# Kernel optimization log

Measured on AMD Instinct MI355X. Metric: run time of the kernel, lower is better.

Reference implementation:

```python
import jax, jax.numpy as jnp
import numpy as np

THETA = 10000.0
NUM_HEADS = 16


def _rope_tables(seq_len, d_k, dtype):
    exponent = jnp.arange(d_k // 2, dtype=jnp.float32) * (2.0 / d_k)
    inv_freq = THETA ** (-exponent)                      # (d_k/2,)
    pos = jnp.arange(seq_len, dtype=jnp.float32)
    angles = pos[:, None] * inv_freq[None, :]            # (n, d_k/2)
    return jnp.cos(angles).astype(dtype), jnp.sin(angles).astype(dtype)


def _apply_rope(x, cos, sin):
    # x: (..., n, d_k); interleaved pair convention: pairs are (x[...,2i], x[...,2i+1])
    x1 = x[..., 0::2]
    x2 = x[..., 1::2]
    r1 = x1 * cos - x2 * sin
    r2 = x1 * sin + x2 * cos
    return jnp.stack([r1, r2], axis=-1).reshape(x.shape)


def setup_inputs() -> dict:
    key = jax.random.key(0)
    ks = jax.random.split(key, 5)
    B, N, D = 2, 4096, 1024
    std = (2.0 / (D + D)) ** 0.5
    return {
        "x": jax.random.normal(ks[0], (B, N, D), dtype=jnp.float32),
        "Wq": jax.random.normal(ks[1], (D, D), dtype=jnp.float32) * std,
        "Wk": jax.random.normal(ks[2], (D, D), dtype=jnp.float32) * std,
        "Wv": jax.random.normal(ks[3], (D, D), dtype=jnp.float32) * std,
        "Wo": jax.random.normal(ks[4], (D, D), dtype=jnp.float32) * std,
    }


def reference(x, Wq, Wk, Wv, Wo):
    B, N, D = x.shape
    H = NUM_HEADS
    d_k = D // H

    def proj(W):
        y = jnp.einsum('oi,bni->bno', W, x)
        return y.reshape(B, N, H, d_k).transpose(0, 2, 1, 3)  # (b,h,n,d)

    Q, K, V = proj(Wq), proj(Wk), proj(Wv)

    cos, sin = _rope_tables(N, d_k, x.dtype)
    Q = _apply_rope(Q, cos, sin)
    K = _apply_rope(K, cos, sin)

    scores = jnp.einsum('bhnd,bhmd->bhnm', Q, K) / jnp.sqrt(jnp.asarray(d_k, x.dtype))
    causal = jnp.tril(jnp.ones((N, N), dtype=bool))
    scores = jnp.where(causal, scores, -jnp.inf)
    attn = jax.nn.softmax(scores, axis=-1)
    out = jnp.einsum('bhnm,bhmd->bhnd', attn, V)          # (b,h,n,d)
    out = out.transpose(0, 2, 1, 3).reshape(B, N, D)
    return jnp.einsum('oi,bni->bno', Wo, out)
```

## Files before the change

kernel.cpp:

```cpp
#include <hip/hip_runtime.h>
#include <hip/hip_bf16.h>
#include <stdint.h>

typedef __attribute__((ext_vector_type(8))) short short8;
typedef __attribute__((ext_vector_type(4))) float f32x4;
typedef __attribute__((ext_vector_type(2))) unsigned uint32x2;

#define NSEQ 4096
#define DMODEL 1024
#define MROWS 8192

__device__ __forceinline__ unsigned short f2bf(float f) {
  union { float f; unsigned u; } v; v.f = f;
  unsigned r = v.u + 0x7fffu + ((v.u >> 16) & 1u);
  return (unsigned short)(r >> 16);
}

__device__ __forceinline__ unsigned pk2(float lo, float hi) {
  unsigned short a = __bfloat16_as_ushort(__float2bfloat16(lo));
  unsigned short b = __bfloat16_as_ushort(__float2bfloat16(hi));
  return ((unsigned)b << 16) | (unsigned)a;
}

__device__ __forceinline__ void gload16(const unsigned short* g, unsigned short* l) {
  __builtin_amdgcn_global_load_lds(
      (const __attribute__((address_space(1))) unsigned int*)g,
      (__attribute__((address_space(3))) unsigned int*)l, 16, 0, 0);
}

__device__ __forceinline__ void pexch(unsigned x, unsigned y, unsigned& w_lo, unsigned& w_hi) {
  uint32x2 t = __builtin_amdgcn_permlane32_swap(x, y, false, false);
  uint32x2 u = __builtin_amdgcn_permlane16_swap(t[0], t[1], false, false);
  w_lo = u[0];
  w_hi = u[1];
}

__global__ void k_conv(const float* __restrict__ src, unsigned short* __restrict__ dst) {
  int i = (blockIdx.x * 256 + threadIdx.x) * 4;
  float4 v = *(const float4*)(src + i);
  ushort4 o;
  o.x = f2bf(v.x); o.y = f2bf(v.y); o.z = f2bf(v.z); o.w = f2bf(v.w);
  *(ushort4*)(dst + i) = o;
}

__global__ void k_convw(const float* __restrict__ s0, const float* __restrict__ s1,
                        const float* __restrict__ s2, const float* __restrict__ s3,
                        unsigned short* __restrict__ dst) {
  int z = blockIdx.x >> 10;
  const float* src = (z == 0) ? s0 : (z == 1) ? s1 : (z == 2) ? s2 : s3;
  float sc = (z == 0) ? 0.18033688011112042f : 1.0f;
  int i = ((blockIdx.x & 1023) * 256 + threadIdx.x) * 4;
  float4 v = *(const float4*)(src + i);
  ushort4 o;
  o.x = f2bf(v.x * sc); o.y = f2bf(v.y * sc); o.z = f2bf(v.z * sc); o.w = f2bf(v.w * sc);
  *(ushort4*)(dst + (size_t)z * 1048576 + i) = o;
}

__global__ void k_rope_tab(float* __restrict__ cosT, float* __restrict__ sinT) {
  int i = blockIdx.x * 256 + threadIdx.x;
  int pos = i >> 5, j = i & 31;
  float invf = exp2f(-(float)j * 0.41524101186092029f);
  float ang = (float)pos * invf;
  cosT[i] = cosf(ang);
  sinT[i] = sinf(ang);
}

__global__ __launch_bounds__(256) void k_gemm_bt(
    const unsigned short* __restrict__ A,
    const unsigned short* __restrict__ Bw,
    unsigned short* __restrict__ obf,
    unsigned short* __restrict__ Vt,
    float* __restrict__ of32,
    const float* __restrict__ cosT, const float* __restrict__ sinT,
    int K, int modeArg) {
  const int N = DMODEL;
  const int q8 = gridDim.x >> 3;
  const int wg = (blockIdx.x & 7) * q8 + (blockIdx.x >> 3);
  const int z = wg >> 9;
  const int rr = wg & 511;
  const int bn = rr & 7, bm = rr >> 3;
  const int mode = (modeArg < 0) ? z : modeArg;
  const unsigned short* Bz = Bw + (size_t)z * DMODEL * K;
  unsigned short* oz = (obf && mode <= 1) ? (obf + (size_t)z * MROWS * DMODEL) : nullptr;

  const int t = threadIdx.x;
  const int w = t >> 6, lane = t & 63;
  const int wr = w >> 1, wc = w & 1;
  const int lr = lane & 15, lg = lane >> 4;

  __shared__ __align__(16) unsigned short SM[2][128 * 64];
  unsigned short* Al = SM[0];
  unsigned short* Bl = SM[1];

  const unsigned short* Ab = A + (size_t)bm * 128 * K;
  const unsigned short* Bb = Bz + (size_t)bn * 128 * K;
  const int trow = t >> 3, tcol = (t & 7) * 8;

  f32x4 acc[4][4] = {};

  for (int k0 = 0; k0 < K; k0 += 64) {
#pragma unroll
    for (int c = 0; c < 4; ++c) {
      gload16(Ab + (size_t)(c * 32 + trow) * K + k0 + tcol, &Al[c * 2048 + t * 8]);
      gload16(Bb + (size_t)(c * 32 + trow) * K + k0 + tcol, &Bl[c * 2048 + t * 8]);
    }
    asm volatile("s_waitcnt vmcnt(0)" ::: "memory");
    __syncthreads();
#pragma unroll
    for (int kk = 0; kk < 2; ++kk) {
      short8 af[4], bfr[4];
#pragma unroll
      for (int mi = 0; mi < 4; ++mi)
        af[mi] = *(const short8*)&Al[(wr * 64 + mi * 16 + lr) * 64 + kk * 32 + lg * 8];
#pragma unroll
      for (int ni = 0; ni < 4; ++ni)
        bfr[ni] = *(const short8*)&Bl[(wc * 64 + ni * 16 + lr) * 64 + kk * 32 + lg * 8];
#pragma unroll
      for (int mi = 0; mi < 4; ++mi)
#pragma unroll
        for (int ni = 0; ni < 4; ++ni)
          acc[mi][ni] = __builtin_amdgcn_mfma_f32_16x16x32_bf16(af[mi], bfr[ni], acc[mi][ni], 0, 0, 0);
    }
    __syncthreads();
  }

  if (mode <= 1 || mode == 3) {
    float* Cf = (float*)&SM[0][0];
#pragma unroll
    for (int half = 0; half < 2; ++half) {
      if (half) __syncthreads();
      if (wr == half) {
#pragma unroll
        for (int mi = 0; mi < 4; ++mi)
#pragma unroll
          for (int ni = 0; ni < 4; ++ni)
#pragma unroll
            for (int r = 0; r < 4; ++r) {
              int row = mi * 16 + lg * 4 + r;
              int col = (wc * 64 + ni * 16 + lr) ^ (lg << 3);
              Cf[row * 128 + col] = acc[mi][ni][r];
            }
      }
      __syncthreads();
      int pr = t >> 2;
      int gm = bm * 128 + half * 64 + pr;
      int xorv = ((pr >> 2) & 3) << 3;
      if (mode == 3) {
        float* orow = of32 + (size_t)gm * N + bn * 128;
#pragma unroll
        for (int k = 0; k < 4; ++k) {
          int c0 = (t & 3) * 8 + k * 32;
          int cs = c0 ^ xorv;
          float4 va = *(const float4*)&Cf[pr * 128 + cs];
          float4 vb = *(const float4*)&Cf[pr * 128 + cs + 4];
          *(float4*)(orow + c0) = va;
          *(float4*)(orow + c0 + 4) = vb;
        }
      } else {
        int pos = gm & (NSEQ - 1);
        const float* cB = cosT + pos * 32;
        const float* sB = sinT + pos * 32;
        unsigned short* orow = oz + (size_t)gm * N + bn * 128;
#pragma unroll
        for (int k = 0; k < 4; ++k) {
          int c0 = (t & 3) * 8 + k * 32;
          int cs = c0 ^ xorv;
          float4 va = *(const float4*)&Cf[pr * 128 + cs];
          float4 vb = *(const float4*)&Cf[pr * 128 + cs + 4];
          int j0 = (c0 & 63) >> 1;
          float4 cv = *(const float4*)&cB[j0];
          float4 sv = *(const float4*)&sB[j0];
          uint4 o;
          o.x = pk2(va.x * cv.x - va.y * sv.x, va.x * sv.x + va.y * cv.x);
          o.y = pk2(va.z * cv.y - va.w * sv.y, va.z * sv.y + va.w * cv.y);
          o.z = pk2(vb.x * cv.z - vb.y * sv.z, vb.x * sv.z + vb.y * cv.z);
          o.w = pk2(vb.z * cv.w - vb.w * sv.w, vb.z * sv.w + vb.w * cv.w);
          *(uint4*)(orow + c0) = o;
        }
      }
    }
  } else {
#pragma unroll
    for (int mi = 0; mi < 4; ++mi)
#pragma unroll
      for (int ni = 0; ni < 4; ++ni) {
        int gm0 = bm * 128 + wr * 64 + mi * 16 + lg * 4;
        int gn = bn * 128 + wc * 64 + ni * 16 + lr;
        int b = gm0 >> 12, n = gm0 & (NSEQ - 1);
        int h = gn >> 6, d = gn & 63;
        uint2 u;
        u.x = pk2(acc[mi][ni][0], acc[mi][ni][1]);
        u.y = pk2(acc[mi][ni][2], acc[mi][ni][3]);
        *(uint2*)(Vt + ((size_t)((b * 16 + h) * 64 + d)) * NSEQ + n) = u;
      }
  }
}

__global__ __launch_bounds__(256, 2) void k_attn8(
    const unsigned short* __restrict__ Qb,
    const unsigned short* __restrict__ Kb,
    const unsigned short* __restrict__ Vtg,
    unsigned short* __restrict__ AO) {
  const int id = blockIdx.x;
  const int bh = id & 31;
  const int pq = id >> 5;
  const int b = bh >> 4, h = bh & 15;
  const int t = threadIdx.x;
  const int w = t >> 6, lane = t & 63;
  const int lr = lane & 15, hi4 = lane >> 4;
  const size_t rowbase = (size_t)b * NSEQ;

  __shared__ __align__(16) unsigned short Kl[2][64 * 64];
  __shared__ __align__(16) unsigned short Vl[2][64 * 64];
  __shared__ __align__(16) unsigned short Pl[4][16 * 64];

  const int pswz = (lr & 7) << 3;

  short8 ones;
#pragma unroll
  for (int i = 0; i < 8; ++i) ones[i] = (short)0x3F80;

#define STAGE(buf, kv0)                                                                   \
  {                                                                                       \
    _Pragma("unroll")                                                                     \
    for (int it = 0; it < 2; ++it) {                                                      \
      int c = t + it * 256;                                                               \
      int row = c >> 3, sg = (c & 7) ^ (row & 7);                                         \
      gload16(Kb + (rowbase + (kv0) + row) * DMODEL + h * 64 + sg * 8, &Kl[buf][c * 8]);  \
      gload16(Vtg + ((size_t)bh * 64 + row) * NSEQ + (kv0) + sg * 8, &Vl[buf][c * 8]);    \
    }                                                                                     \
  }

#pragma unroll
  for (int qi = 0; qi < 2; ++qi) {
    const int qt = qi ? pq : (31 - pq);
    const int q0w = qt * 128 + w * 32;

    short8 qf[2][2];
#pragma unroll
    for (int sub = 0; sub < 2; ++sub) {
      const unsigned short* qp = Qb + (rowbase + q0w + sub * 16 + lr) * DMODEL + h * 64 + hi4 * 8;
#pragma unroll
      for (int s = 0; s < 2; ++s)
        qf[sub][s] = *(const short8*)(qp + s * 32);
    }

    f32x4 oacc[2][4] = {};
    f32x4 lacc[2] = {};
    const int nkv = (qt + 1) * 2;

    STAGE(0, 0);
    asm volatile("s_waitcnt vmcnt(0)" ::: "memory");
    __syncthreads();

    for (int ib = 0; ib < nkv; ++ib) {
      const int kv0 = ib * 64, cur = ib & 1;
      if (ib + 1 < nkv) STAGE(cur ^ 1, kv0 + 64);

      if (kv0 <= q0w + 31) {
        short8 Kf[4][2], Vf[2][4];
#pragma unroll
        for (int t4 = 0; t4 < 4; ++t4)
#pragma unroll
          for (int s = 0; s < 2; ++s)
            Kf[t4][s] = *(const short8*)&Kl[cur][(t4 * 16 + lr) * 64 + (((s * 4 + hi4) ^ (lr & 7)) * 8)];
#pragma unroll
        for (int c = 0; c < 2; ++c)
#pragma unroll
          for (int dt = 0; dt < 4; ++dt)
            Vf[c][dt] = *(const short8*)&Vl[cur][(dt * 16 + lr) * 64 + (((c * 4 + hi4) ^ (lr & 7)) * 8)];

#pragma unroll
        for (int sub = 0; sub < 2; ++sub) {
          const int qs = q0w + sub * 16;
          const int qlane = qs + lr;
          f32x4 sa[4];
          const f32x4 zz = {0.f, 0.f, 0.f, 0.f};
          __builtin_amdgcn_s_setprio(1);
#pragma unroll
          for (int t4 = 0; t4 < 4; ++t4) {
            f32x4 x = __builtin_amdgcn_mfma_f32_16x16x32_bf16(Kf[t4][0], qf[sub][0], zz, 0, 0, 0);
            sa[t4] = __builtin_amdgcn_mfma_f32_16x16x32_bf16(Kf[t4][1], qf[sub][1], x, 0, 0, 0);
          }
          __builtin_amdgcn_s_setprio(0);
          if (kv0 + 63 > qs) {
#pragma unroll
            for (int t4 = 0; t4 < 4; ++t4)
#pragma unroll
              for (int r = 0; r < 4; ++r)
                if (kv0 + t4 * 16 + hi4 * 4 + r > qlane) sa[t4][r] = -1e30f;
          }
#pragma unroll
          for (int t4 = 0; t4 < 4; ++t4)
#pragma unroll
            for (int r = 0; r < 4; ++r)
              sa[t4][r] = __builtin_amdgcn_exp2f(sa[t4][r]);

          unsigned a0 = pk2(sa[0][0], sa[0][1]), a1 = pk2(sa[0][2], sa[0][3]);
          unsigned a2 = pk2(sa[1][0], sa[1][1]), a3 = pk2(sa[1][2], sa[1][3]);
          unsigned a4 = pk2(sa[2][0], sa[2][1]), a5 = pk2(sa[2][2], sa[2][3]);
          unsigned a6 = pk2(sa[3][0], sa[3][1]), a7 = pk2(sa[3][2], sa[3][3]);
          unsigned w0, w1, w2, w3, x0, x1, x2, x3;
          pexch(a0, a2, w0, w2);
          pexch(a1, a3, w1, w3);
          pexch(a4, a6, x0, x2);
          pexch(a5, a7, x1, x3);
          union { uint4 u; short8 s; } P0, P1;
          P0.u.x = w0; P0.u.y = w1; P0.u.z = w2; P0.u.w = w3;
          P1.u.x = x0; P1.u.y = x1; P1.u.z = x2; P1.u.w = x3;
          short8 pf0 = P0.s;
          short8 pf1 = P1.s;

          __builtin_amdgcn_s_setprio(1);
#pragma unroll
          for (int dt = 0; dt < 4; ++dt) {
            oacc[sub][dt] = __builtin_amdgcn_mfma_f32_16x16x32_bf16(Vf[0][dt], pf0, oacc[sub][dt], 0, 0, 0);
            oacc[sub][dt] = __builtin_amdgcn_mfma_f32_16x16x32_bf16(Vf[1][dt], pf1, oacc[sub][dt], 0, 0, 0);
          }
          lacc[sub] = __builtin_amdgcn_mfma_f32_16x16x32_bf16(ones, pf0, lacc[sub], 0, 0, 0);
          lacc[sub] = __builtin_amdgcn_mfma_f32_16x16x32_bf16(ones, pf1, lacc[sub], 0, 0, 0);
          __builtin_amdgcn_s_setprio(0);
        }
      }
      asm volatile("s_waitcnt vmcnt(0)" ::: "memory");
      __syncthreads();
    }

#pragma unroll
    for (int sub = 0; sub < 2; ++sub) {
      float inv = 1.f / lacc[sub][0];
#pragma unroll
      for (int dt = 0; dt < 4; ++dt) {
        uint2 u;
        u.x = pk2(oacc[sub][dt][0] * inv, oacc[sub][dt][1] * inv);
        u.y = pk2(oacc[sub][dt][2] * inv, oacc[sub][dt][3] * inv);
        *(uint2*)&Pl[w][lr * 64 + ((dt * 16 + hi4 * 4) ^ pswz)] = u;
      }
      asm volatile("s_waitcnt lgkmcnt(0)" ::: "memory");
      __builtin_amdgcn_sched_barrier(0);
      int q2 = lane >> 2, ch = (lane & 3) * 16;
      int qswz = (q2 & 7) << 3;
      uint4 r0 = *(const uint4*)&Pl[w][q2 * 64 + (ch ^ qswz)];
      uint4 r1 = *(const uint4*)&Pl[w][q2 * 64 + ((ch + 8) ^ qswz)];
      unsigned short* op = AO + (rowbase + q0w + sub * 16 + q2) * DMODEL + h * 64 + ch;
      *(uint4*)op = r0;
      *(uint4*)(op + 8) = r1;
      __syncthreads();
    }
  }
}

extern "C" void kernel_launch(void* const* d_in, const int* in_sizes, int n_in,
                              void* d_out, int out_size, void* d_ws, size_t ws_size,
                              hipStream_t stream) {
  const float* x  = (const float*)d_in[0];
  const float* Wq = (const float*)d_in[1];
  const float* Wk = (const float*)d_in[2];
  const float* Wv = (const float*)d_in[3];
  const float* Wo = (const float*)d_in[4];
  float* out = (float*)d_out;
  char* ws = (char*)d_ws;

  unsigned short* xb  = (unsigned short*)(ws);
  unsigned short* Wb  = (unsigned short*)(ws + 16777216);
  unsigned short* Qb  = (unsigned short*)(ws + 25165824);
  unsigned short* Kb  = Qb + 8388608;
  unsigned short* Vtg = (unsigned short*)(ws + 58720256);
  unsigned short* AO  = (unsigned short*)(ws + 75497472);
  float* cosT = (float*)(ws + 92274688);
  float* sinT = (float*)(ws + 92798976);

  k_conv<<<8192, 256, 0, stream>>>(x, xb);
  k_convw<<<4096, 256, 0, stream>>>(Wq, Wk, Wv, Wo, Wb);
  k_rope_tab<<<512, 256, 0, stream>>>(cosT, sinT);

  k_gemm_bt<<<1536, 256, 0, stream>>>(xb, Wb, Qb, Vtg, nullptr, cosT, sinT, DMODEL, -1);

  k_attn8<<<512, 256, 0, stream>>>(Qb, Kb, Vtg, AO);

  k_gemm_bt<<<512, 256, 0, stream>>>(AO, Wb + 3145728, nullptr, nullptr, out, cosT, sinT, DMODEL, 3);
}
```

Measured before the change: 226.7 us.

## Use 256-row query tiles per attention block to raise K/V reuse

The attention kernel now gives each block one 256-row query tile (64 rows per wave) instead of two paired 128-row tiles. Each staged 64-row K/V tile therefore serves twice as many query rows, which halves shared-memory staging and global K/V traffic. Heavy tiles are dispatched first to soften the causal load imbalance. The costs are more accumulator and P-fragment registers and idle waves on the diagonal tiles. The bf16 packing helper also switches to a manual round-to-nearest-even conversion.

```diff
diff --git a/kernel.cpp b/kernel.cpp
--- a/kernel.cpp
+++ b/kernel.cpp
@@ -17,9 +17,7 @@
 }
 
 __device__ __forceinline__ unsigned pk2(float lo, float hi) {
-  unsigned short a = __bfloat16_as_ushort(__float2bfloat16(lo));
-  unsigned short b = __bfloat16_as_ushort(__float2bfloat16(hi));
-  return ((unsigned)b << 16) | (unsigned)a;
+  return ((unsigned)f2bf(hi) << 16) | (unsigned)f2bf(lo);
 }
 
 __device__ __forceinline__ void gload16(const unsigned short* g, unsigned short* l) {
@@ -196,18 +194,19 @@
   }
 }
 
-__global__ __launch_bounds__(256, 2) void k_attn8(
+__global__ __launch_bounds__(256, 2) void k_attn10(
     const unsigned short* __restrict__ Qb,
     const unsigned short* __restrict__ Kb,
     const unsigned short* __restrict__ Vtg,
     unsigned short* __restrict__ AO) {
   const int id = blockIdx.x;
   const int bh = id & 31;
-  const int pq = id >> 5;
+  const int qt = 15 - (id >> 5);
   const int b = bh >> 4, h = bh & 15;
   const int t = threadIdx.x;
   const int w = t >> 6, lane = t & 63;
   const int lr = lane & 15, hi4 = lane >> 4;
+  const int q0 = qt * 256 + w * 64;
   const size_t rowbase = (size_t)b * NSEQ;
 
   __shared__ __align__(16) unsigned short Kl[2][64 * 64];
@@ -231,122 +230,123 @@
     }                                                                                     \
   }
 
-#pragma unroll
-  for (int qi = 0; qi < 2; ++qi) {
-    const int qt = qi ? pq : (31 - pq);
-    const int q0w = qt * 128 + w * 32;
-
-    short8 qf[2][2];
-#pragma unroll
-    for (int sub = 0; sub < 2; ++sub) {
-      const unsigned short* qp = Qb + (rowbase + q0w + sub * 16 + lr) * DMODEL + h * 64 + hi4 * 8;
-#pragma unroll
-      for (int s = 0; s < 2; ++s)
-        qf[sub][s] = *(const short8*)(qp + s * 32);
-    }
-
-    f32x4 oacc[2][4] = {};
-    f32x4 lacc[2] = {};
-    const int nkv = (qt + 1) * 2;
-
-    STAGE(0, 0);
+  short8 qf[4][2];
+#pragma unroll
+  for (int sub = 0; sub < 4; ++sub) {
+    const unsigned short* qp = Qb + (rowbase + q0 + sub * 16 + lr) * DMODEL + h * 64 + hi4 * 8;
+#pragma unroll
+    for (int s = 0; s < 2; ++s)
+      qf[sub][s] = *(const short8*)(qp + s * 32);
+  }
+
+  f32x4 oacc[4][4] = {};
+  f32x4 lacc[4] = {};
+  const int nkv = (qt + 1) * 4;
+
+  STAGE(0, 0);
+  asm volatile("s_waitcnt vmcnt(0)" ::: "memory");
+  __syncthreads();
+
+  for (int ib = 0; ib < nkv; ++ib) {
+    const int kv0 = ib * 64, cur = ib & 1;
+    if (ib + 1 < nkv) STAGE(cur ^ 1, kv0 + 64);
+
+    if (kv0 <= q0 + 63) {
+      short8 Kf[4][2];
+#pragma unroll
+      for (int t4 = 0; t4 < 4; ++t4)
+#pragma unroll
+        for (int s = 0; s < 2; ++s)
+          Kf[t4][s] = *(const short8*)&Kl[cur][(t4 * 16 + lr) * 64 + (((s * 4 + hi4) ^ (lr & 7)) * 8)];
+
+      short8 pf[4][2];
+#pragma unroll
+      for (int sub = 0; sub < 4; ++sub) {
+        const int qs = q0 + sub * 16;
+        const int qlane = qs + lr;
+        f32x4 sa[4];
+        const f32x4 zz = {0.f, 0.f, 0.f, 0.f};
+        __builtin_amdgcn_s_setprio(1);
+#pragma unroll
+        for (int t4 = 0; t4 < 4; ++t4) {
+          f32x4 x = __builtin_amdgcn_mfma_f32_16x16x32_bf16(Kf[t4][0], qf[sub][0], zz, 0, 0, 0);
+          sa[t4] = __builtin_amdgcn_mfma_f32_16x16x32_bf16(Kf[t4][1], qf[sub][1], x, 0, 0, 0);
+        }
+        __builtin_amdgcn_s_setprio(0);
+        if (kv0 + 63 > qs) {
+#pragma unroll
+          for (int t4 = 0; t4 < 4; ++t4)
+#pragma unroll
+            for (int r = 0; r < 4; ++r)
+              if (kv0 + t4 * 16 + hi4 * 4 + r > qlane) sa[t4][r] = -1e30f;
+        }
+#pragma unroll
+        for (int t4 = 0; t4 < 4; ++t4)
+#pragma unroll
+          for (int r = 0; r < 4; ++r)
+            sa[t4][r] = __builtin_amdgcn_exp2f(sa[t4][r]);
+
+        unsigned a0 = pk2(sa[0][0], sa[0][1]), a1 = pk2(sa[0][2], sa[0][3]);
+        unsigned a2 = pk2(sa[1][0], sa[1][1]), a3 = pk2(sa[1][2], sa[1][3]);
+        unsigned a4 = pk2(sa[2][0], sa[2][1]), a5 = pk2(sa[2][2], sa[2][3]);
+        unsigned a6 = pk2(sa[3][0], sa[3][1]), a7 = pk2(sa[3][2], sa[3][3]);
+        unsigned w0, w1, w2, w3, x0, x1, x2, x3;
+        pexch(a0, a2, w0, w2);
+        pexch(a1, a3, w1, w3);
+        pexch(a4, a6, x0, x2);
+        pexch(a5, a7, x1, x3);
+        union { uint4 u; short8 s; } P0, P1;
+        P0.u.x = w0; P0.u.y = w1; P0.u.z = w2; P0.u.w = w3;
+        P1.u.x = x0; P1.u.y = x1; P1.u.z = x2; P1.u.w = x3;
+        pf[sub][0] = P0.s;
+        pf[sub][1] = P1.s;
+      }
+
+      short8 Vf[2][4];
+#pragma unroll
+      for (int c = 0; c < 2; ++c)
+#pragma unroll
+        for (int dt = 0; dt < 4; ++dt)
+          Vf[c][dt] = *(const short8*)&Vl[cur][(dt * 16 + lr) * 64 + (((c * 4 + hi4) ^ (lr & 7)) * 8)];
+
+      __builtin_amdgcn_s_setprio(1);
+#pragma unroll
+      for (int sub = 0; sub < 4; ++sub) {
+#pragma unroll
+        for (int dt = 0; dt < 4; ++dt) {
+          oacc[sub][dt] = __builtin_amdgcn_mfma_f32_16x16x32_bf16(Vf[0][dt], pf[sub][0], oacc[sub][dt], 0, 0, 0);
+          oacc[sub][dt] = __builtin_amdgcn_mfma_f32_16x16x32_bf16(Vf[1][dt], pf[sub][1], oacc[sub][dt], 0, 0, 0);
+        }
+        lacc[sub] = __builtin_amdgcn_mfma_f32_16x16x32_bf16(ones, pf[sub][0], lacc[sub], 0, 0, 0);
+        lacc[sub] = __builtin_amdgcn_mfma_f32_16x16x32_bf16(ones, pf[sub][1], lacc[sub], 0, 0, 0);
+      }
+      __builtin_amdgcn_s_setprio(0);
+    }
     asm volatile("s_waitcnt vmcnt(0)" ::: "memory");
     __syncthreads();
-
-    for (int ib = 0; ib < nkv; ++ib) {
-      const int kv0 = ib * 64, cur = ib & 1;
-      if (ib + 1 < nkv) STAGE(cur ^ 1, kv0 + 64);
-
-      if (kv0 <= q0w + 31) {
-        short8 Kf[4][2], Vf[2][4];
-#pragma unroll
-        for (int t4 = 0; t4 < 4; ++t4)
-#pragma unroll
-          for (int s = 0; s < 2; ++s)
-            Kf[t4][s] = *(const short8*)&Kl[cur][(t4 * 16 + lr) * 64 + (((s * 4 + hi4) ^ (lr & 7)) * 8)];
-#pragma unroll
-        for (int c = 0; c < 2; ++c)
-#pragma unroll
-          for (int dt = 0; dt < 4; ++dt)
-            Vf[c][dt] = *(const short8*)&Vl[cur][(dt * 16 + lr) * 64 + (((c * 4 + hi4) ^ (lr & 7)) * 8)];
-
-#pragma unroll
-        for (int sub = 0; sub < 2; ++sub) {
-          const int qs = q0w + sub * 16;
-          const int qlane = qs + lr;
-          f32x4 sa[4];
-          const f32x4 zz = {0.f, 0.f, 0.f, 0.f};
-          __builtin_amdgcn_s_setprio(1);
-#pragma unroll
-          for (int t4 = 0; t4 < 4; ++t4) {
-            f32x4 x = __builtin_amdgcn_mfma_f32_16x16x32_bf16(Kf[t4][0], qf[sub][0], zz, 0, 0, 0);
-            sa[t4] = __builtin_amdgcn_mfma_f32_16x16x32_bf16(Kf[t4][1], qf[sub][1], x, 0, 0, 0);
-          }
-          __builtin_amdgcn_s_setprio(0);
-          if (kv0 + 63 > qs) {
-#pragma unroll
-            for (int t4 = 0; t4 < 4; ++t4)
-#pragma unroll
-              for (int r = 0; r < 4; ++r)
-                if (kv0 + t4 * 16 + hi4 * 4 + r > qlane) sa[t4][r] = -1e30f;
-          }
-#pragma unroll
-          for (int t4 = 0; t4 < 4; ++t4)
-#pragma unroll
-            for (int r = 0; r < 4; ++r)
-              sa[t4][r] = __builtin_amdgcn_exp2f(sa[t4][r]);
-
-          unsigned a0 = pk2(sa[0][0], sa[0][1]), a1 = pk2(sa[0][2], sa[0][3]);
-          unsigned a2 = pk2(sa[1][0], sa[1][1]), a3 = pk2(sa[1][2], sa[1][3]);
-          unsigned a4 = pk2(sa[2][0], sa[2][1]), a5 = pk2(sa[2][2], sa[2][3]);
-          unsigned a6 = pk2(sa[3][0], sa[3][1]), a7 = pk2(sa[3][2], sa[3][3]);
-          unsigned w0, w1, w2, w3, x0, x1, x2, x3;
-          pexch(a0, a2, w0, w2);
-          pexch(a1, a3, w1, w3);
-          pexch(a4, a6, x0, x2);
-          pexch(a5, a7, x1, x3);
-          union { uint4 u; short8 s; } P0, P1;
-          P0.u.x = w0; P0.u.y = w1; P0.u.z = w2; P0.u.w = w3;
-          P1.u.x = x0; P1.u.y = x1; P1.u.z = x2; P1.u.w = x3;
-          short8 pf0 = P0.s;
-          short8 pf1 = P1.s;
-
-          __builtin_amdgcn_s_setprio(1);
-#pragma unroll
-          for (int dt = 0; dt < 4; ++dt) {
-            oacc[sub][dt] = __builtin_amdgcn_mfma_f32_16x16x32_bf16(Vf[0][dt], pf0, oacc[sub][dt], 0, 0, 0);
-            oacc[sub][dt] = __builtin_amdgcn_mfma_f32_16x16x32_bf16(Vf[1][dt], pf1, oacc[sub][dt], 0, 0, 0);
-          }
-          lacc[sub] = __builtin_amdgcn_mfma_f32_16x16x32_bf16(ones, pf0, lacc[sub], 0, 0, 0);
-          lacc[sub] = __builtin_amdgcn_mfma_f32_16x16x32_bf16(ones, pf1, lacc[sub], 0, 0, 0);
-          __builtin_amdgcn_s_setprio(0);
-        }
-      }
-      asm volatile("s_waitcnt vmcnt(0)" ::: "memory");
-      __syncthreads();
-    }
-
-#pragma unroll
-    for (int sub = 0; sub < 2; ++sub) {
-      float inv = 1.f / lacc[sub][0];
-#pragma unroll
-      for (int dt = 0; dt < 4; ++dt) {
-        uint2 u;
-        u.x = pk2(oacc[sub][dt][0] * inv, oacc[sub][dt][1] * inv);
-        u.y = pk2(oacc[sub][dt][2] * inv, oacc[sub][dt][3] * inv);
-        *(uint2*)&Pl[w][lr * 64 + ((dt * 16 + hi4 * 4) ^ pswz)] = u;
-      }
-      asm volatile("s_waitcnt lgkmcnt(0)" ::: "memory");
-      __builtin_amdgcn_sched_barrier(0);
-      int q2 = lane >> 2, ch = (lane & 3) * 16;
-      int qswz = (q2 & 7) << 3;
-      uint4 r0 = *(const uint4*)&Pl[w][q2 * 64 + (ch ^ qswz)];
-      uint4 r1 = *(const uint4*)&Pl[w][q2 * 64 + ((ch + 8) ^ qswz)];
-      unsigned short* op = AO + (rowbase + q0w + sub * 16 + q2) * DMODEL + h * 64 + ch;
-      *(uint4*)op = r0;
-      *(uint4*)(op + 8) = r1;
-      __syncthreads();
-    }
+  }
+
+#pragma unroll
+  for (int sub = 0; sub < 4; ++sub) {
+    float inv = 1.f / lacc[sub][0];
+#pragma unroll
+    for (int dt = 0; dt < 4; ++dt) {
+      uint2 u;
+      u.x = pk2(oacc[sub][dt][0] * inv, oacc[sub][dt][1] * inv);
+      u.y = pk2(oacc[sub][dt][2] * inv, oacc[sub][dt][3] * inv);
+      *(uint2*)&Pl[w][lr * 64 + ((dt * 16 + hi4 * 4) ^ pswz)] = u;
+    }
+    asm volatile("s_waitcnt lgkmcnt(0)" ::: "memory");
+    __builtin_amdgcn_sched_barrier(0);
+    int q2 = lane >> 2, ch = (lane & 3) * 16;
+    int qswz = (q2 & 7) << 3;
+    uint4 r0 = *(const uint4*)&Pl[w][q2 * 64 + (ch ^ qswz)];
+    uint4 r1 = *(const uint4*)&Pl[w][q2 * 64 + ((ch + 8) ^ qswz)];
+    unsigned short* op = AO + (rowbase + q0 + sub * 16 + q2) * DMODEL + h * 64 + ch;
+    *(uint4*)op = r0;
+    *(uint4*)(op + 8) = r1;
+    asm volatile("s_waitcnt lgkmcnt(0)" ::: "memory");
+    __builtin_amdgcn_sched_barrier(0);
   }
 }
 
@@ -376,7 +376,7 @@
 
   k_gemm_bt<<<1536, 256, 0, stream>>>(xb, Wb, Qb, Vtg, nullptr, cosT, sinT, DMODEL, -1);
 
-  k_attn8<<<512, 256, 0, stream>>>(Qb, Kb, Vtg, AO);
+  k_attn10<<<512, 256, 0, stream>>>(Qb, Kb, Vtg, AO);
 
   k_gemm_bt<<<512, 256, 0, stream>>>(AO, Wb + 3145728, nullptr, nullptr, out, cosT, sinT, DMODEL, 3);
 }
```

Measured after the change: 258.9 us. 1.14x slower.

## Restructure attention into 512-thread blocks covering 256-query tiles

Applied to the files above, without the earlier changes.

The attention kernel now uses 8 waves per block, each block owning one 256-row query tile. Previously a 4-wave block processed two 128-row tiles one after another, paired for load balance. Each K/V tile staged in LDS is now shared by twice as many query rows, cutting global K/V traffic and per-tile staging overhead, and the sequential two-tile loop goes away. Causal balance now comes from pairing adjacent blocks (qt and 15-qt) instead of work inside one block, which risks wave imbalance and lower occupancy at the larger block size. The bf16 pack also switches to a manual round-to-nearest-even helper.

```diff
diff --git a/kernel.cpp b/kernel.cpp
--- a/kernel.cpp
+++ b/kernel.cpp
@@ -17,9 +17,7 @@
 }
 
 __device__ __forceinline__ unsigned pk2(float lo, float hi) {
-  unsigned short a = __bfloat16_as_ushort(__float2bfloat16(lo));
-  unsigned short b = __bfloat16_as_ushort(__float2bfloat16(hi));
-  return ((unsigned)b << 16) | (unsigned)a;
+  return ((unsigned)f2bf(hi) << 16) | (unsigned)f2bf(lo);
 }
 
 __device__ __forceinline__ void gload16(const unsigned short* g, unsigned short* l) {
@@ -196,23 +194,26 @@
   }
 }
 
-__global__ __launch_bounds__(256, 2) void k_attn8(
+__global__ __launch_bounds__(512, 2) void k_attn11(
     const unsigned short* __restrict__ Qb,
     const unsigned short* __restrict__ Kb,
     const unsigned short* __restrict__ Vtg,
     unsigned short* __restrict__ AO) {
   const int id = blockIdx.x;
-  const int bh = id & 31;
-  const int pq = id >> 5;
+  const int p = id >> 1, odd = id & 1;
+  const int bh = p & 31;
+  const int pq = p >> 5;
+  const int qt = odd ? pq : 15 - pq;
   const int b = bh >> 4, h = bh & 15;
   const int t = threadIdx.x;
   const int w = t >> 6, lane = t & 63;
   const int lr = lane & 15, hi4 = lane >> 4;
+  const int q0 = qt * 256 + w * 32;
   const size_t rowbase = (size_t)b * NSEQ;
 
   __shared__ __align__(16) unsigned short Kl[2][64 * 64];
   __shared__ __align__(16) unsigned short Vl[2][64 * 64];
-  __shared__ __align__(16) unsigned short Pl[4][16 * 64];
+  __shared__ __align__(16) unsigned short Pl[8][16 * 64];
 
   const int pswz = (lr & 7) << 3;
 
@@ -220,133 +221,125 @@
 #pragma unroll
   for (int i = 0; i < 8; ++i) ones[i] = (short)0x3F80;
 
-#define STAGE(buf, kv0)                                                                   \
-  {                                                                                       \
-    _Pragma("unroll")                                                                     \
-    for (int it = 0; it < 2; ++it) {                                                      \
-      int c = t + it * 256;                                                               \
-      int row = c >> 3, sg = (c & 7) ^ (row & 7);                                         \
-      gload16(Kb + (rowbase + (kv0) + row) * DMODEL + h * 64 + sg * 8, &Kl[buf][c * 8]);  \
-      gload16(Vtg + ((size_t)bh * 64 + row) * NSEQ + (kv0) + sg * 8, &Vl[buf][c * 8]);    \
-    }                                                                                     \
-  }
-
-#pragma unroll
-  for (int qi = 0; qi < 2; ++qi) {
-    const int qt = qi ? pq : (31 - pq);
-    const int q0w = qt * 128 + w * 32;
-
-    short8 qf[2][2];
-#pragma unroll
-    for (int sub = 0; sub < 2; ++sub) {
-      const unsigned short* qp = Qb + (rowbase + q0w + sub * 16 + lr) * DMODEL + h * 64 + hi4 * 8;
-#pragma unroll
-      for (int s = 0; s < 2; ++s)
-        qf[sub][s] = *(const short8*)(qp + s * 32);
-    }
-
-    f32x4 oacc[2][4] = {};
-    f32x4 lacc[2] = {};
-    const int nkv = (qt + 1) * 2;
-
-    STAGE(0, 0);
+  const int srow = t >> 3, sg = ((t & 7) ^ (srow & 7)) * 8;
+
+#define STAGE(buf, kv0)                                                                 \
+  {                                                                                     \
+    gload16(Kb + (rowbase + (kv0) + srow) * DMODEL + h * 64 + sg, &Kl[buf][t * 8]);     \
+    gload16(Vtg + ((size_t)bh * 64 + srow) * NSEQ + (kv0) + sg, &Vl[buf][t * 8]);       \
+  }
+
+  short8 qf[2][2];
+#pragma unroll
+  for (int sub = 0; sub < 2; ++sub) {
+    const unsigned short* qp = Qb + (rowbase + q0 + sub * 16 + lr) * DMODEL + h * 64 + hi4 * 8;
+#pragma unroll
+    for (int s = 0; s < 2; ++s)
+      qf[sub][s] = *(const short8*)(qp + s * 32);
+  }
+
+  f32x4 oacc[2][4] = {};
+  f32x4 lacc[2] = {};
+  const int nkv = (qt + 1) * 4;
+
+  STAGE(0, 0);
+  asm volatile("s_waitcnt vmcnt(0)" ::: "memory");
+  __syncthreads();
+
+  for (int ib = 0; ib < nkv; ++ib) {
+    const int kv0 = ib * 64, cur = ib & 1;
+    if (ib + 1 < nkv) STAGE(cur ^ 1, kv0 + 64);
+
+    if (kv0 <= q0 + 31) {
+      short8 Kf[4][2], Vf[2][4];
+#pragma unroll
+      for (int t4 = 0; t4 < 4; ++t4)
+#pragma unroll
+        for (int s = 0; s < 2; ++s)
+          Kf[t4][s] = *(const short8*)&Kl[cur][(t4 * 16 + lr) * 64 + (((s * 4 + hi4) ^ (lr & 7)) * 8)];
+#pragma unroll
+      for (int c = 0; c < 2; ++c)
+#pragma unroll
+        for (int dt = 0; dt < 4; ++dt)
+          Vf[c][dt] = *(const short8*)&Vl[cur][(dt * 16 + lr) * 64 + (((c * 4 + hi4) ^ (lr & 7)) * 8)];
+
+#pragma unroll
+      for (int sub = 0; sub < 2; ++sub) {
+        const int qs = q0 + sub * 16;
+        const int qlane = qs + lr;
+        f32x4 sa[4];
+        const f32x4 zz = {0.f, 0.f, 0.f, 0.f};
+        __builtin_amdgcn_s_setprio(1);
+#pragma unroll
+        for (int t4 = 0; t4 < 4; ++t4) {
+          f32x4 x = __builtin_amdgcn_mfma_f32_16x16x32_bf16(Kf[t4][0], qf[sub][0], zz, 0, 0, 0);
+          sa[t4] = __builtin_amdgcn_mfma_f32_16x16x32_bf16(Kf[t4][1], qf[sub][1], x, 0, 0, 0);
+        }
+        __builtin_amdgcn_s_setprio(0);
+        if (kv0 + 63 > qs) {
+#pragma unroll
+          for (int t4 = 0; t4 < 4; ++t4)
+#pragma unroll
+            for (int r = 0; r < 4; ++r)
+              if (kv0 + t4 * 16 + hi4 * 4 + r > qlane) sa[t4][r] = -1e30f;
+        }
+#pragma unroll
+        for (int t4 = 0; t4 < 4; ++t4)
+#pragma unroll
+          for (int r = 0; r < 4; ++r)
+            sa[t4][r] = __builtin_amdgcn_exp2f(sa[t4][r]);
+
+        unsigned a0 = pk2(sa[0][0], sa[0][1]), a1 = pk2(sa[0][2], sa[0][3]);
+        unsigned a2 = pk2(sa[1][0], sa[1][1]), a3 = pk2(sa[1][2], sa[1][3]);
+        unsigned a4 = pk2(sa[2][0], sa[2][1]), a5 = pk2(sa[2][2], sa[2][3]);
+        unsigned a6 = pk2(sa[3][0], sa[3][1]), a7 = pk2(sa[3][2], sa[3][3]);
+        unsigned w0, w1, w2, w3, x0, x1, x2, x3;
+        pexch(a0, a2, w0, w2);
+        pexch(a1, a3, w1, w3);
+        pexch(a4, a6, x0, x2);
+        pexch(a5, a7, x1, x3);
+        union { uint4 u; short8 s; } P0, P1;
+        P0.u.x = w0; P0.u.y = w1; P0.u.z = w2; P0.u.w = w3;
+        P1.u.x = x0; P1.u.y = x1; P1.u.z = x2; P1.u.w = x3;
+        short8 pf0 = P0.s;
+        short8 pf1 = P1.s;
+
+        __builtin_amdgcn_s_setprio(1);
+#pragma unroll
+        for (int dt = 0; dt < 4; ++dt) {
+          oacc[sub][dt] = __builtin_amdgcn_mfma_f32_16x16x32_bf16(Vf[0][dt], pf0, oacc[sub][dt], 0, 0, 0);
+          oacc[sub][dt] = __builtin_amdgcn_mfma_f32_16x16x32_bf16(Vf[1][dt], pf1, oacc[sub][dt], 0, 0, 0);
+        }
+        lacc[sub] = __builtin_amdgcn_mfma_f32_16x16x32_bf16(ones, pf0, lacc[sub], 0, 0, 0);
+        lacc[sub] = __builtin_amdgcn_mfma_f32_16x16x32_bf16(ones, pf1, lacc[sub], 0, 0, 0);
+        __builtin_amdgcn_s_setprio(0);
+      }
+    }
     asm volatile("s_waitcnt vmcnt(0)" ::: "memory");
     __syncthreads();
-
-    for (int ib = 0; ib < nkv; ++ib) {
-      const int kv0 = ib * 64, cur = ib & 1;
-      if (ib + 1 < nkv) STAGE(cur ^ 1, kv0 + 64);
-
-      if (kv0 <= q0w + 31) {
-        short8 Kf[4][2], Vf[2][4];
-#pragma unroll
-        for (int t4 = 0; t4 < 4; ++t4)
-#pragma unroll
-          for (int s = 0; s < 2; ++s)
-            Kf[t4][s] = *(const short8*)&Kl[cur][(t4 * 16 + lr) * 64 + (((s * 4 + hi4) ^ (lr & 7)) * 8)];
-#pragma unroll
-        for (int c = 0; c < 2; ++c)
-#pragma unroll
-          for (int dt = 0; dt < 4; ++dt)
-            Vf[c][dt] = *(const short8*)&Vl[cur][(dt * 16 + lr) * 64 + (((c * 4 + hi4) ^ (lr & 7)) * 8)];
-
-#pragma unroll
-        for (int sub = 0; sub < 2; ++sub) {
-          const int qs = q0w + sub * 16;
-          const int qlane = qs + lr;
-          f32x4 sa[4];
-          const f32x4 zz = {0.f, 0.f, 0.f, 0.f};
-          __builtin_amdgcn_s_setprio(1);
-#pragma unroll
-          for (int t4 = 0; t4 < 4; ++t4) {
-            f32x4 x = __builtin_amdgcn_mfma_f32_16x16x32_bf16(Kf[t4][0], qf[sub][0], zz, 0, 0, 0);
-            sa[t4] = __builtin_amdgcn_mfma_f32_16x16x32_bf16(Kf[t4][1], qf[sub][1], x, 0, 0, 0);
-          }
-          __builtin_amdgcn_s_setprio(0);
-          if (kv0 + 63 > qs) {
-#pragma unroll
-            for (int t4 = 0; t4 < 4; ++t4)
-#pragma unroll
-              for (int r = 0; r < 4; ++r)
-                if (kv0 + t4 * 16 + hi4 * 4 + r > qlane) sa[t4][r] = -1e30f;
-          }
-#pragma unroll
-          for (int t4 = 0; t4 < 4; ++t4)
-#pragma unroll
-            for (int r = 0; r < 4; ++r)
-              sa[t4][r] = __builtin_amdgcn_exp2f(sa[t4][r]);
-
-          unsigned a0 = pk2(sa[0][0], sa[0][1]), a1 = pk2(sa[0][2], sa[0][3]);
-          unsigned a2 = pk2(sa[1][0], sa[1][1]), a3 = pk2(sa[1][2], sa[1][3]);
-          unsigned a4 = pk2(sa[2][0], sa[2][1]), a5 = pk2(sa[2][2], sa[2][3]);
-          unsigned a6 = pk2(sa[3][0], sa[3][1]), a7 = pk2(sa[3][2], sa[3][3]);
-          unsigned w0, w1, w2, w3, x0, x1, x2, x3;
-          pexch(a0, a2, w0, w2);
-          pexch(a1, a3, w1, w3);
-          pexch(a4, a6, x0, x2);
-          pexch(a5, a7, x1, x3);
-          union { uint4 u; short8 s; } P0, P1;
-          P0.u.x = w0; P0.u.y = w1; P0.u.z = w2; P0.u.w = w3;
-          P1.u.x = x0; P1.u.y = x1; P1.u.z = x2; P1.u.w = x3;
-          short8 pf0 = P0.s;
-          short8 pf1 = P1.s;
-
-          __builtin_amdgcn_s_setprio(1);
-#pragma unroll
-          for (int dt = 0; dt < 4; ++dt) {
-            oacc[sub][dt] = __builtin_amdgcn_mfma_f32_16x16x32_bf16(Vf[0][dt], pf0, oacc[sub][dt], 0, 0, 0);
-            oacc[sub][dt] = __builtin_amdgcn_mfma_f32_16x16x32_bf16(Vf[1][dt], pf1, oacc[sub][dt], 0, 0, 0);
-          }
-          lacc[sub] = __builtin_amdgcn_mfma_f32_16x16x32_bf16(ones, pf0, lacc[sub], 0, 0, 0);
-          lacc[sub] = __builtin_amdgcn_mfma_f32_16x16x32_bf16(ones, pf1, lacc[sub], 0, 0, 0);
-          __builtin_amdgcn_s_setprio(0);
-        }
-      }
-      asm volatile("s_waitcnt vmcnt(0)" ::: "memory");
-      __syncthreads();
-    }
-
-#pragma unroll
-    for (int sub = 0; sub < 2; ++sub) {
-      float inv = 1.f / lacc[sub][0];
-#pragma unroll
-      for (int dt = 0; dt < 4; ++dt) {
-        uint2 u;
-        u.x = pk2(oacc[sub][dt][0] * inv, oacc[sub][dt][1] * inv);
-        u.y = pk2(oacc[sub][dt][2] * inv, oacc[sub][dt][3] * inv);
-        *(uint2*)&Pl[w][lr * 64 + ((dt * 16 + hi4 * 4) ^ pswz)] = u;
-      }
-      asm volatile("s_waitcnt lgkmcnt(0)" ::: "memory");
-      __builtin_amdgcn_sched_barrier(0);
-      int q2 = lane >> 2, ch = (lane & 3) * 16;
-      int qswz = (q2 & 7) << 3;
-      uint4 r0 = *(const uint4*)&Pl[w][q2 * 64 + (ch ^ qswz)];
-      uint4 r1 = *(const uint4*)&Pl[w][q2 * 64 + ((ch + 8) ^ qswz)];
-      unsigned short* op = AO + (rowbase + q0w + sub * 16 + q2) * DMODEL + h * 64 + ch;
-      *(uint4*)op = r0;
-      *(uint4*)(op + 8) = r1;
-      __syncthreads();
-    }
+  }
+
+#pragma unroll
+  for (int sub = 0; sub < 2; ++sub) {
+    float inv = 1.f / lacc[sub][0];
+#pragma unroll
+    for (int dt = 0; dt < 4; ++dt) {
+      uint2 u;
+      u.x = pk2(oacc[sub][dt][0] * inv, oacc[sub][dt][1] * inv);
+      u.y = pk2(oacc[sub][dt][2] * inv, oacc[sub][dt][3] * inv);
+      *(uint2*)&Pl[w][lr * 64 + ((dt * 16 + hi4 * 4) ^ pswz)] = u;
+    }
+    asm volatile("s_waitcnt lgkmcnt(0)" ::: "memory");
+    __builtin_amdgcn_sched_barrier(0);
+    int q2 = lane >> 2, ch = (lane & 3) * 16;
+    int qswz = (q2 & 7) << 3;
+    uint4 r0 = *(const uint4*)&Pl[w][q2 * 64 + (ch ^ qswz)];
+    uint4 r1 = *(const uint4*)&Pl[w][q2 * 64 + ((ch + 8) ^ qswz)];
+    unsigned short* op = AO + (rowbase + q0 + sub * 16 + q2) * DMODEL + h * 64 + ch;
+    *(uint4*)op = r0;
+    *(uint4*)(op + 8) = r1;
+    asm volatile("s_waitcnt lgkmcnt(0)" ::: "memory");
+    __builtin_amdgcn_sched_barrier(0);
   }
 }
 
@@ -376,7 +369,7 @@
 
   k_gemm_bt<<<1536, 256, 0, stream>>>(xb, Wb, Qb, Vtg, nullptr, cosT, sinT, DMODEL, -1);
 
-  k_attn8<<<512, 256, 0, stream>>>(Qb, Kb, Vtg, AO);
+  k_attn11<<<512, 512, 0, stream>>>(Qb, Kb, Vtg, AO);
 
   k_gemm_bt<<<512, 256, 0, stream>>>(AO, Wb + 3145728, nullptr, nullptr, out, cosT, sinT, DMODEL, 3);
 }
```

After: 310.7 us. 37.0% more time.
